# Optimization experiments

Hardware: AMD Instinct MI355X
Metric: run time of the kernel (lower is better)

The kernel has to match this reference:

```python
import jax, jax.numpy as jnp
from jax import lax
import numpy as np

B, T = 32, 64
E = 64        # embed_dim
U = 32        # num_measurements
D0, D1 = 300, 100
S = 9         # speaker_num
CELL = 64     # output_cell_dim
C = 6         # n_classes
EPS = 1e-12


def setup_inputs() -> dict:
    key = jax.random.key(0)
    ks = jax.random.split(key, 16)
    sc = 1.0 / np.sqrt(E)
    n = lambda i, shape, s=1.0: (jax.random.normal(ks[i], shape, jnp.float32) * s)
    return {
        "x0": n(0, (B, T, D0)),
        "x1": n(1, (B, T, D1)),
        "smask": jax.random.uniform(ks[2], (B, T, S), jnp.float32),
        "umask": jnp.ones((B, T), jnp.float32),
        "W_ih0": n(3, (4 * E, D0), sc), "W_hh0": n(4, (4 * E, E), sc),
        "b_ih0": n(5, (4 * E,), sc), "b_hh0": n(6, (4 * E,), sc),
        "W_ih1": n(7, (4 * E, D1), sc), "W_hh1": n(8, (4 * E, E), sc),
        "b_ih1": n(9, (4 * E,), sc), "b_hh1": n(10, (4 * E,), sc),
        "phase_table": jax.random.uniform(ks[11], (S, E), jnp.float32, -np.pi, np.pi),
        "meas_kernel": jax.random.uniform(ks[12], (U, E, 2), jnp.float32),
        "W1": n(13, (CELL, 2 * U), 0.1), "b1": jnp.zeros((CELL,), jnp.float32),
        "W2": n(14, (C, CELL), 0.1), "b2": jnp.zeros((C,), jnp.float32),
    }


def _lstm_tanh(x, um, Wih, Whh, bih, bhh):
    # torch.nn.LSTMCell (gate order i,f,g,o) + extra tanh applied to h each step;
    # the tanh-ed h is carried as the recurrent state (dropout = identity in eval).
    b, t, _ = x.shape
    e = Whh.shape[1]

    def step(carry, inp):
        h, c = carry
        xt, ut = inp
        g = (xt * ut[:, None]) @ Wih.T + bih + h @ Whh.T + bhh
        i, f, gg, o = jnp.split(g, 4, axis=-1)
        c = jax.nn.sigmoid(f) * c + jax.nn.sigmoid(i) * jnp.tanh(gg)
        h = jnp.tanh(jax.nn.sigmoid(o) * jnp.tanh(c))
        return (h, c), h

    h0 = jnp.zeros((b, e), x.dtype)
    _, hs = lax.scan(step, (h0, h0), (jnp.swapaxes(x, 0, 1), um.T))
    return jnp.swapaxes(hs, 0, 1)  # (B,T,E)


def _measure(amp, phase, kernel):
    # pure state v = cos(phase)*amp + i sin(phase)*amp; rho = |v><v|
    r = jnp.cos(phase) * amp
    im = jnp.sin(phase) * amp
    rho_r = jnp.einsum('bti,btj->btij', r, r) + jnp.einsum('bti,btj->btij', im, im)
    rho_i = jnp.einsum('bti,btj->btij', im, r) - jnp.einsum('bti,btj->btij', r, im)
    u = kernel.shape[0]
    norm = jnp.clip(jnp.linalg.norm(kernel.reshape(u, -1), axis=-1), EPS)
    kn = kernel / norm[:, None, None]
    kr, ki = kn[..., 0], kn[..., 1]
    Pr = jnp.einsum('ui,uj->uij', kr, kr) + jnp.einsum('ui,uj->uij', ki, ki)
    Pi = jnp.einsum('ui,uj->uij', ki, kr) - jnp.einsum('ui,uj->uij', kr, ki)
    return jnp.einsum('btij,uij->btu', rho_r, Pr) - jnp.einsum('btij,uij->btu', rho_i, Pi)


def reference(x0, x1, smask, umask, W_ih0, W_hh0, b_ih0, b_hh0,
              W_ih1, W_hh1, b_ih1, b_hh1, phase_table, meas_kernel,
              W1, b1, W2, b2):
    h0 = _lstm_tanh(x0, umask, W_ih0, W_hh0, b_ih0, b_hh0)
    h1 = _lstm_tanh(x1, umask, W_ih1, W_hh1, b_ih1, b_hh1)
    norm = lambda h: h / jnp.clip(jnp.linalg.norm(h, axis=-1, keepdims=True), EPS)
    phase = phase_table[jnp.argmax(smask, axis=-1)]  # (B,T,E); table shared by both modalities
    m = jnp.concatenate([_measure(norm(h0), phase, meas_kernel),
                         _measure(norm(h1), phase, meas_kernel)], axis=-1)
    hid = jax.nn.relu(m @ W1.T + b1)
    pred = jnp.tanh(hid @ W2.T + b2)
    return jax.nn.log_softmax(pred, axis=2)
```

## Files before the change

### kernel.cpp

```cpp
#include <hip/hip_runtime.h>

typedef unsigned short ushort_t;
typedef unsigned int uint_t;

__device__ __forceinline__ float bf2f(ushort_t v) {
  union { uint_t u; float f; } x; x.u = ((uint_t)v) << 16; return x.f;
}
__device__ __forceinline__ float lo16(uint_t u) {
  union { uint_t u; float f; } x; x.u = u << 16; return x.f;
}
__device__ __forceinline__ float hi16(uint_t u) {
  union { uint_t u; float f; } x; x.u = u & 0xffff0000u; return x.f;
}
__device__ __forceinline__ ushort_t f2bf(float f) {
  union { float f; uint_t u; } x; x.f = f;
  uint_t u = x.u;
  uint_t r = (u + 0x7fffu + ((u >> 16) & 1u)) >> 16;
  return (ushort_t)r;
}
__device__ __forceinline__ bool is_bf16(const void* um) {
  return *(const uint_t*)um == 0x3F803F80u;
}
__device__ __forceinline__ float ld_dual(const void* p, int i, bool isb) {
  return isb ? bf2f(((const ushort_t*)p)[i]) : ((const float*)p)[i];
}
__device__ __forceinline__ float fsig(float x) { return 1.f / (1.f + __expf(-x)); }
__device__ __forceinline__ float ftanh(float x) { return 2.f / (1.f + __expf(-2.f * x)) - 1.f; }

__device__ __forceinline__ float dpp_add_xor1(float v) {
  const int r = __builtin_amdgcn_update_dpp(0, __float_as_int(v), 0xB1, 0xF, 0xF, true);
  return v + __int_as_float(r);
}
__device__ __forceinline__ float dpp_add_xor2(float v) {
  const int r = __builtin_amdgcn_update_dpp(0, __float_as_int(v), 0x4E, 0xF, 0xF, true);
  return v + __int_as_float(r);
}

template <int D, bool ISB>
__device__ __forceinline__ void proj_body(
    const void* __restrict__ x, const void* __restrict__ um,
    const void* __restrict__ Wih, const void* __restrict__ bih,
    const void* __restrict__ bhh, float* __restrict__ xw, float* xs)
{
  const int tid = threadIdx.x;
  const int r0 = blockIdx.x * 8;
  for (int i = tid; i < 8 * D; i += 256) {
    const int r = i / D;
    xs[i] = ld_dual(x, r0 * D + i, ISB) * ld_dual(um, r0 + r, ISB);
  }
  __syncthreads();
  float acc[8];
#pragma unroll
  for (int r = 0; r < 8; ++r) acc[r] = 0.f;
#pragma unroll 5
  for (int k = 0; k < D; k += 4) {
    float w0, w1, w2, w3;
    if (ISB) {
      const ushort_t* wr = (const ushort_t*)Wih + tid * D;
      const uint2 wu = *(const uint2*)(wr + k);
      w0 = lo16(wu.x); w1 = hi16(wu.x); w2 = lo16(wu.y); w3 = hi16(wu.y);
    } else {
      const float* wr = (const float*)Wih + tid * D;
      const float4 wv = *(const float4*)(wr + k);
      w0 = wv.x; w1 = wv.y; w2 = wv.z; w3 = wv.w;
    }
#pragma unroll
    for (int r = 0; r < 8; ++r) {
      const float4 xv = *(const float4*)(xs + r * D + k);
      acc[r] = fmaf(xv.x, w0, acc[r]);
      acc[r] = fmaf(xv.y, w1, acc[r]);
      acc[r] = fmaf(xv.z, w2, acc[r]);
      acc[r] = fmaf(xv.w, w3, acc[r]);
    }
  }
  const float bias = ld_dual(bih, tid, ISB) + ld_dual(bhh, tid, ISB);
  const int pos = ((tid & 63) << 2) | (tid >> 6);
#pragma unroll
  for (int r = 0; r < 8; ++r)
    xw[(r0 + r) * 256 + pos] = acc[r] + bias;
}

__global__ __launch_bounds__(256) void proj_both(
    const void* __restrict__ x0, const void* __restrict__ x1,
    const void* __restrict__ um,
    const void* __restrict__ Wih0, const void* __restrict__ bih0,
    const void* __restrict__ bhh0,
    const void* __restrict__ Wih1, const void* __restrict__ bih1,
    const void* __restrict__ bhh1,
    float* __restrict__ xw0, float* __restrict__ xw1)
{
  __shared__ __align__(16) float xs[8 * 300];
  const bool isb = is_bf16(um);
  if (blockIdx.y == 0) {
    if (isb) proj_body<300, true>(x0, um, Wih0, bih0, bhh0, xw0, xs);
    else     proj_body<300, false>(x0, um, Wih0, bih0, bhh0, xw0, xs);
  } else {
    if (isb) proj_body<100, true>(x1, um, Wih1, bih1, bhh1, xw1, xs);
    else     proj_body<100, false>(x1, um, Wih1, bih1, bhh1, xw1, xs);
  }
}

__global__ __launch_bounds__(256, 1) void lstm_k(
    const float* __restrict__ xw0, const float* __restrict__ xw1,
    const void* __restrict__ Whh0, const void* __restrict__ Whh1,
    const void* __restrict__ um,
    float* __restrict__ h0r, float* __restrict__ h1r)
{
  __shared__ __align__(16) float xws[64 * 256];
  __shared__ __align__(16) float hist[65 * 64];

  const int bid = blockIdx.x;
  const int l = bid >> 5;
  const int b = bid & 31;
  const float* xw = (l ? xw1 : xw0) + b * 64 * 256;
  const void* Whh = (l ? Whh1 : Whh0);
  float* hr = (l ? h1r : h0r) + b * 64 * 64;
  const int tid = threadIdx.x;
  const int e = tid >> 2;
  const int q = tid & 3;
  const int k0 = q << 4;
  const bool isb = is_bf16(um);

  for (int i = tid; i < 4096; i += 256)
    *(float4*)(xws + i * 4) = *(const float4*)(xw + i * 4);
  if (tid < 64) hist[tid] = 0.f;

  float w[4][16];
  if (isb) {
#pragma unroll
    for (int t = 0; t < 4; ++t) {
      const ushort_t* wr = (const ushort_t*)Whh + (t * 64 + e) * 64 + k0;
#pragma unroll
      for (int j = 0; j < 16; j += 8) {
        const uint4 v = *(const uint4*)(wr + j);
        w[t][j + 0] = lo16(v.x); w[t][j + 1] = hi16(v.x);
        w[t][j + 2] = lo16(v.y); w[t][j + 3] = hi16(v.y);
        w[t][j + 4] = lo16(v.z); w[t][j + 5] = hi16(v.z);
        w[t][j + 6] = lo16(v.w); w[t][j + 7] = hi16(v.w);
      }
    }
  } else {
#pragma unroll
    for (int t = 0; t < 4; ++t) {
      const float* wr = (const float*)Whh + (t * 64 + e) * 64 + k0;
#pragma unroll
      for (int j = 0; j < 16; j += 4) {
        const float4 v = *(const float4*)(wr + j);
        w[t][j + 0] = v.x; w[t][j + 1] = v.y;
        w[t][j + 2] = v.z; w[t][j + 3] = v.w;
      }
    }
  }
  __syncthreads();

  float c = 0.f;
  for (int s = 0; s < 64; ++s) {
    const float gin = xws[s * 256 + tid];
    const float* hp = hist + s * 64 + k0;
    float p0 = 0.f, p1 = 0.f, p2 = 0.f, p3 = 0.f;
#pragma unroll
    for (int j = 0; j < 16; j += 4) {
      const float4 hv = *(const float4*)(hp + j);
      p0 = fmaf(w[0][j + 0], hv.x, p0); p0 = fmaf(w[0][j + 1], hv.y, p0);
      p0 = fmaf(w[0][j + 2], hv.z, p0); p0 = fmaf(w[0][j + 3], hv.w, p0);
      p1 = fmaf(w[1][j + 0], hv.x, p1); p1 = fmaf(w[1][j + 1], hv.y, p1);
      p1 = fmaf(w[1][j + 2], hv.z, p1); p1 = fmaf(w[1][j + 3], hv.w, p1);
      p2 = fmaf(w[2][j + 0], hv.x, p2); p2 = fmaf(w[2][j + 1], hv.y, p2);
      p2 = fmaf(w[2][j + 2], hv.z, p2); p2 = fmaf(w[2][j + 3], hv.w, p2);
      p3 = fmaf(w[3][j + 0], hv.x, p3); p3 = fmaf(w[3][j + 1], hv.y, p3);
      p3 = fmaf(w[3][j + 2], hv.z, p3); p3 = fmaf(w[3][j + 3], hv.w, p3);
    }
    if (q == 0) p0 += gin;
    else if (q == 1) p1 += gin;
    else if (q == 2) p2 += gin;
    else p3 += gin;
    p0 = dpp_add_xor1(p0); p0 = dpp_add_xor2(p0);
    p1 = dpp_add_xor1(p1); p1 = dpp_add_xor2(p1);
    p2 = dpp_add_xor1(p2); p2 = dpp_add_xor2(p2);
    p3 = dpp_add_xor1(p3); p3 = dpp_add_xor2(p3);
    const float yi = fsig(p0);
    const float yf = fsig(p1);
    const float yg = ftanh(p2);
    const float yo = fsig(p3);
    c = fmaf(yf, c, yi * yg);
    const float h = ftanh(yo * ftanh(c));
    if (q == 0) hist[(s + 1) * 64 + e] = h;
    __syncthreads();
  }
  for (int i = tid; i < 1024; i += 256)
    *(float4*)(hr + i * 4) = *(const float4*)(hist + 64 + i * 4);
}

__global__ __launch_bounds__(256) void head_k(
    const float* __restrict__ h0r, const float* __restrict__ h1r,
    const void* __restrict__ smask, const void* __restrict__ um,
    const void* __restrict__ ptab, const void* __restrict__ mker,
    const void* __restrict__ W1, const void* __restrict__ b1,
    const void* __restrict__ W2, const void* __restrict__ b2,
    void* __restrict__ out)
{
  __shared__ float2 knT[64][32];
  __shared__ float w1T[64][64];
  __shared__ float w2T[64][8];
  __shared__ float b1s[64];
  __shared__ float b2s[8];
  __shared__ float rim[4][4][64];
  __shared__ float msh[4][64];
  __shared__ float hidsh[4][64];
  __shared__ float psh[4][8];

  const int tid = threadIdx.x;
  const bool isb = is_bf16(um);
  {
    const int u = tid >> 3, sub = tid & 7;
    float vr[8], vi[8];
    float ssq = 0.f;
#pragma unroll
    for (int qq = 0; qq < 8; ++qq) {
      const int e = sub * 8 + qq;
      if (isb) {
        const uint_t kk = ((const uint_t*)mker)[u * 64 + e];
        vr[qq] = lo16(kk); vi[qq] = hi16(kk);
      } else {
        const float2 kk = ((const float2*)mker)[u * 64 + e];
        vr[qq] = kk.x; vi[qq] = kk.y;
      }
      ssq = fmaf(vr[qq], vr[qq], ssq);
      ssq = fmaf(vi[qq], vi[qq], ssq);
    }
    ssq += __shfl_xor(ssq, 1);
    ssq += __shfl_xor(ssq, 2);
    ssq += __shfl_xor(ssq, 4);
    const float rn = 1.f / fmaxf(sqrtf(ssq), 1e-12f);
#pragma unroll
    for (int qq = 0; qq < 8; ++qq) {
      const int e = sub * 8 + qq;
      knT[e][u] = make_float2(vr[qq] * rn, vi[qq] * rn);
    }
  }
  for (int i = tid; i < 4096; i += 256) {
    const int j = i >> 6, ll = i & 63;
    w1T[ll][j] = ld_dual(W1, i, isb);
  }
  if (tid < 64) b1s[tid] = ld_dual(b1, tid, isb);
  for (int i = tid; i < 384; i += 256) {
    const int cc = i >> 6, j = i & 63;
    w2T[j][cc] = ld_dual(W2, i, isb);
  }
  if (tid < 6) b2s[tid] = ld_dual(b2, tid, isb);
  __syncthreads();

  const int wv = tid >> 6, lane = tid & 63;
  const int item = blockIdx.x * 4 + wv;
  const float h0raw = h0r[item * 64 + lane];
  const float h1raw = h1r[item * 64 + lane];
  float ss0 = h0raw * h0raw, ss1 = h1raw * h1raw;
#pragma unroll
  for (int m = 1; m < 64; m <<= 1) {
    ss0 += __shfl_xor(ss0, m);
    ss1 += __shfl_xor(ss1, m);
  }
  const float h0 = h0raw / fmaxf(sqrtf(ss0), 1e-12f);
  const float h1 = h1raw / fmaxf(sqrtf(ss1), 1e-12f);

  int idx = 0;
  if (lane == 0) {
    float best = -1e30f;
#pragma unroll
    for (int si = 0; si < 9; ++si) {
      const float v = ld_dual(smask, item * 9 + si, isb);
      if (v > best) { best = v; idx = si; }
    }
  }
  idx = __shfl(idx, 0, 64);
  const float ph = ld_dual(ptab, idx * 64 + lane, isb);
  float sr, cr;
  __sincosf(ph, &sr, &cr);
  rim[wv][0][lane] = cr * h0;
  rim[wv][1][lane] = sr * h0;
  rim[wv][2][lane] = cr * h1;
  rim[wv][3][lane] = sr * h1;
  __syncthreads();
  {
    const int u = lane & 31;
    const float* ra = rim[wv][(lane >= 32) ? 2 : 0];
    const float* ia = rim[wv][(lane >= 32) ? 3 : 1];
    float ar = 0.f, ai = 0.f;
#pragma unroll 8
    for (int e = 0; e < 64; ++e) {
      const float2 k = knT[e][u];
      const float rr = ra[e], ii = ia[e];
      ar = fmaf(rr, k.x, ar);
      ar = fmaf(-ii, k.y, ar);
      ai = fmaf(rr, k.y, ai);
      ai = fmaf(ii, k.x, ai);
    }
    msh[wv][lane] = fmaf(ar, ar, ai * ai);
  }
  __syncthreads();
  {
    float acc = b1s[lane];
#pragma unroll 8
    for (int L = 0; L < 64; ++L)
      acc = fmaf(msh[wv][L], w1T[L][lane], acc);
    hidsh[wv][lane] = fmaxf(acc, 0.f);
  }
  __syncthreads();
  if (lane < 6) {
    float a2 = b2s[lane];
#pragma unroll 8
    for (int j = 0; j < 64; ++j)
      a2 = fmaf(hidsh[wv][j], w2T[j][lane], a2);
    psh[wv][lane] = ftanh(a2);
  }
  __syncthreads();
  if (lane < 6) {
    const float p = psh[wv][lane];
    float mx = psh[wv][0];
#pragma unroll
    for (int cc = 1; cc < 6; ++cc) mx = fmaxf(mx, psh[wv][cc]);
    float sum = 0.f;
#pragma unroll
    for (int cc = 0; cc < 6; ++cc) sum += __expf(psh[wv][cc] - mx);
    const float res = p - mx - __logf(sum);
    if (isb) ((ushort_t*)out)[item * 6 + lane] = f2bf(res);
    else     ((float*)out)[item * 6 + lane] = res;
  }
}

extern "C" void kernel_launch(void* const* d_in, const int* in_sizes, int n_in,
                              void* d_out, int out_size, void* d_ws, size_t ws_size,
                              hipStream_t stream)
{
  (void)in_sizes; (void)n_in; (void)out_size; (void)ws_size;
  const void* x0    = d_in[0];
  const void* x1    = d_in[1];
  const void* smask = d_in[2];
  const void* um    = d_in[3];
  const void* Wih0  = d_in[4];
  const void* Whh0  = d_in[5];
  const void* bih0  = d_in[6];
  const void* bhh0  = d_in[7];
  const void* Wih1  = d_in[8];
  const void* Whh1  = d_in[9];
  const void* bih1  = d_in[10];
  const void* bhh1  = d_in[11];
  const void* ptab  = d_in[12];
  const void* mker  = d_in[13];
  const void* W1    = d_in[14];
  const void* b1    = d_in[15];
  const void* W2    = d_in[16];
  const void* b2    = d_in[17];

  float* xw0 = (float*)d_ws;
  float* xw1 = xw0 + 2048 * 256;
  float* h0r = xw1 + 2048 * 256;
  float* h1r = h0r + 2048 * 64;

  hipLaunchKernelGGL(proj_both, dim3(256, 2), dim3(256), 0, stream,
                     x0, x1, um, Wih0, bih0, bhh0, Wih1, bih1, bhh1,
                     xw0, xw1);
  hipLaunchKernelGGL(lstm_k, dim3(64), dim3(256), 0, stream,
                     xw0, xw1, Whh0, Whh1, um, h0r, h1r);
  hipLaunchKernelGGL(head_k, dim3(512), dim3(256), 0, stream,
                     h0r, h1r, smask, um, ptab, mker, W1, b1, W2, b2,
                     d_out);
}
```

Baseline: 165.9 us.

## Use packed 2-wide FMA in LSTM and input projection, retile projection blocks

Rewrites the inner products of the recurrent LSTM step and the input projection to use 2-wide float vectors with an elementwise fma builtin, aiming for packed FP32 FMA instructions on CDNA. The projection kernel now uses 512-thread blocks covering 16 rows, with each thread computing two gate outputs over four rows, so fewer blocks are launched and each weight load is reused more. The head kernel's shared weight arrays are padded to avoid bank conflicts. Packed FMA changes the summation order slightly, and the larger projection blocks may lower occupancy.

```diff
diff --git a/kernel.cpp b/kernel.cpp
--- a/kernel.cpp
+++ b/kernel.cpp
@@ -2,6 +2,7 @@
 
 typedef unsigned short ushort_t;
 typedef unsigned int uint_t;
+typedef float f32x2 __attribute__((ext_vector_type(2)));
 
 __device__ __forceinline__ float bf2f(ushort_t v) {
   union { uint_t u; float f; } x; x.u = ((uint_t)v) << 16; return x.f;
@@ -27,6 +28,18 @@
 __device__ __forceinline__ float fsig(float x) { return 1.f / (1.f + __expf(-x)); }
 __device__ __forceinline__ float ftanh(float x) { return 2.f / (1.f + __expf(-2.f * x)) - 1.f; }
 
+#if defined(__has_builtin)
+#if __has_builtin(__builtin_elementwise_fma)
+#define FMA2(a, b, c) __builtin_elementwise_fma((a), (b), (c))
+#endif
+#endif
+#ifndef FMA2
+__device__ __forceinline__ f32x2 fma2_fb(f32x2 a, f32x2 b, f32x2 c) {
+  c.x = fmaf(a.x, b.x, c.x); c.y = fmaf(a.y, b.y, c.y); return c;
+}
+#define FMA2(a, b, c) fma2_fb((a), (b), (c))
+#endif
+
 __device__ __forceinline__ float dpp_add_xor1(float v) {
   const int r = __builtin_amdgcn_update_dpp(0, __float_as_int(v), 0xB1, 0xF, 0xF, true);
   return v + __int_as_float(r);
@@ -43,44 +56,59 @@
     const void* __restrict__ bhh, float* __restrict__ xw, float* xs)
 {
   const int tid = threadIdx.x;
-  const int r0 = blockIdx.x * 8;
-  for (int i = tid; i < 8 * D; i += 256) {
+  const int gp = tid & 127;
+  const int rg4 = (tid >> 7) << 2;
+  const int r0 = blockIdx.x * 16;
+  for (int i = tid; i < 16 * D; i += 512) {
     const int r = i / D;
     xs[i] = ld_dual(x, r0 * D + i, ISB) * ld_dual(um, r0 + r, ISB);
   }
   __syncthreads();
-  float acc[8];
-#pragma unroll
-  for (int r = 0; r < 8; ++r) acc[r] = 0.f;
+  f32x2 acc[2][4];
+#pragma unroll
+  for (int g = 0; g < 2; ++g)
+#pragma unroll
+    for (int r = 0; r < 4; ++r) acc[g][r] = f32x2{0.f, 0.f};
 #pragma unroll 5
   for (int k = 0; k < D; k += 4) {
-    float w0, w1, w2, w3;
+    f32x2 wA0, wA1, wB0, wB1;
     if (ISB) {
-      const ushort_t* wr = (const ushort_t*)Wih + tid * D;
-      const uint2 wu = *(const uint2*)(wr + k);
-      w0 = lo16(wu.x); w1 = hi16(wu.x); w2 = lo16(wu.y); w3 = hi16(wu.y);
+      const ushort_t* w0p = (const ushort_t*)Wih + (2 * gp) * D + k;
+      const uint2 u0 = *(const uint2*)w0p;
+      const uint2 u1 = *(const uint2*)(w0p + D);
+      wA0 = f32x2{lo16(u0.x), hi16(u0.x)}; wA1 = f32x2{lo16(u0.y), hi16(u0.y)};
+      wB0 = f32x2{lo16(u1.x), hi16(u1.x)}; wB1 = f32x2{lo16(u1.y), hi16(u1.y)};
     } else {
-      const float* wr = (const float*)Wih + tid * D;
-      const float4 wv = *(const float4*)(wr + k);
-      w0 = wv.x; w1 = wv.y; w2 = wv.z; w3 = wv.w;
-    }
-#pragma unroll
-    for (int r = 0; r < 8; ++r) {
-      const float4 xv = *(const float4*)(xs + r * D + k);
-      acc[r] = fmaf(xv.x, w0, acc[r]);
-      acc[r] = fmaf(xv.y, w1, acc[r]);
-      acc[r] = fmaf(xv.z, w2, acc[r]);
-      acc[r] = fmaf(xv.w, w3, acc[r]);
-    }
-  }
-  const float bias = ld_dual(bih, tid, ISB) + ld_dual(bhh, tid, ISB);
-  const int pos = ((tid & 63) << 2) | (tid >> 6);
-#pragma unroll
-  for (int r = 0; r < 8; ++r)
-    xw[(r0 + r) * 256 + pos] = acc[r] + bias;
-}
-
-__global__ __launch_bounds__(256) void proj_both(
+      const float* w0p = (const float*)Wih + (2 * gp) * D + k;
+      const float4 f0 = *(const float4*)w0p;
+      const float4 f1 = *(const float4*)(w0p + D);
+      wA0 = f32x2{f0.x, f0.y}; wA1 = f32x2{f0.z, f0.w};
+      wB0 = f32x2{f1.x, f1.y}; wB1 = f32x2{f1.z, f1.w};
+    }
+#pragma unroll
+    for (int r = 0; r < 4; ++r) {
+      const float4 xv = *(const float4*)(xs + (rg4 + r) * D + k);
+      const f32x2 xA = {xv.x, xv.y}, xB = {xv.z, xv.w};
+      acc[0][r] = FMA2(xA, wA0, acc[0][r]);
+      acc[0][r] = FMA2(xB, wA1, acc[0][r]);
+      acc[1][r] = FMA2(xA, wB0, acc[1][r]);
+      acc[1][r] = FMA2(xB, wB1, acc[1][r]);
+    }
+  }
+  const int g0 = 2 * gp, g1 = 2 * gp + 1;
+  const float b0 = ld_dual(bih, g0, ISB) + ld_dual(bhh, g0, ISB);
+  const float b1v = ld_dual(bih, g1, ISB) + ld_dual(bhh, g1, ISB);
+  const int pos0 = ((g0 & 63) << 2) | (g0 >> 6);
+  const int pos1 = ((g1 & 63) << 2) | (g1 >> 6);
+#pragma unroll
+  for (int r = 0; r < 4; ++r) {
+    const int row = r0 + rg4 + r;
+    xw[row * 256 + pos0] = acc[0][r].x + acc[0][r].y + b0;
+    xw[row * 256 + pos1] = acc[1][r].x + acc[1][r].y + b1v;
+  }
+}
+
+__global__ __launch_bounds__(512) void proj_both(
     const void* __restrict__ x0, const void* __restrict__ x1,
     const void* __restrict__ um,
     const void* __restrict__ Wih0, const void* __restrict__ bih0,
@@ -89,7 +117,7 @@
     const void* __restrict__ bhh1,
     float* __restrict__ xw0, float* __restrict__ xw1)
 {
-  __shared__ __align__(16) float xs[8 * 300];
+  __shared__ __align__(16) float xs[16 * 300];
   const bool isb = is_bf16(um);
   if (blockIdx.y == 0) {
     if (isb) proj_body<300, true>(x0, um, Wih0, bih0, bhh0, xw0, xs);
@@ -125,7 +153,7 @@
     *(float4*)(xws + i * 4) = *(const float4*)(xw + i * 4);
   if (tid < 64) hist[tid] = 0.f;
 
-  float w[4][16];
+  f32x2 w2[4][8];
   if (isb) {
 #pragma unroll
     for (int t = 0; t < 4; ++t) {
@@ -133,10 +161,10 @@
 #pragma unroll
       for (int j = 0; j < 16; j += 8) {
         const uint4 v = *(const uint4*)(wr + j);
-        w[t][j + 0] = lo16(v.x); w[t][j + 1] = hi16(v.x);
-        w[t][j + 2] = lo16(v.y); w[t][j + 3] = hi16(v.y);
-        w[t][j + 4] = lo16(v.z); w[t][j + 5] = hi16(v.z);
-        w[t][j + 6] = lo16(v.w); w[t][j + 7] = hi16(v.w);
+        w2[t][(j >> 1) + 0] = f32x2{lo16(v.x), hi16(v.x)};
+        w2[t][(j >> 1) + 1] = f32x2{lo16(v.y), hi16(v.y)};
+        w2[t][(j >> 1) + 2] = f32x2{lo16(v.z), hi16(v.z)};
+        w2[t][(j >> 1) + 3] = f32x2{lo16(v.w), hi16(v.w)};
       }
     }
   } else {
@@ -146,8 +174,8 @@
 #pragma unroll
       for (int j = 0; j < 16; j += 4) {
         const float4 v = *(const float4*)(wr + j);
-        w[t][j + 0] = v.x; w[t][j + 1] = v.y;
-        w[t][j + 2] = v.z; w[t][j + 3] = v.w;
+        w2[t][(j >> 1) + 0] = f32x2{v.x, v.y};
+        w2[t][(j >> 1) + 1] = f32x2{v.z, v.w};
       }
     }
   }
@@ -157,19 +185,21 @@
   for (int s = 0; s < 64; ++s) {
     const float gin = xws[s * 256 + tid];
     const float* hp = hist + s * 64 + k0;
-    float p0 = 0.f, p1 = 0.f, p2 = 0.f, p3 = 0.f;
+    f32x2 P0 = {0.f, 0.f}, P1 = {0.f, 0.f}, P2 = {0.f, 0.f}, P3 = {0.f, 0.f};
 #pragma unroll
     for (int j = 0; j < 16; j += 4) {
       const float4 hv = *(const float4*)(hp + j);
-      p0 = fmaf(w[0][j + 0], hv.x, p0); p0 = fmaf(w[0][j + 1], hv.y, p0);
-      p0 = fmaf(w[0][j + 2], hv.z, p0); p0 = fmaf(w[0][j + 3], hv.w, p0);
-      p1 = fmaf(w[1][j + 0], hv.x, p1); p1 = fmaf(w[1][j + 1], hv.y, p1);
-      p1 = fmaf(w[1][j + 2], hv.z, p1); p1 = fmaf(w[1][j + 3], hv.w, p1);
-      p2 = fmaf(w[2][j + 0], hv.x, p2); p2 = fmaf(w[2][j + 1], hv.y, p2);
-      p2 = fmaf(w[2][j + 2], hv.z, p2); p2 = fmaf(w[2][j + 3], hv.w, p2);
-      p3 = fmaf(w[3][j + 0], hv.x, p3); p3 = fmaf(w[3][j + 1], hv.y, p3);
-      p3 = fmaf(w[3][j + 2], hv.z, p3); p3 = fmaf(w[3][j + 3], hv.w, p3);
-    }
+      const f32x2 hA = {hv.x, hv.y}, hB = {hv.z, hv.w};
+      const int jp = j >> 1;
+      P0 = FMA2(w2[0][jp], hA, P0); P0 = FMA2(w2[0][jp + 1], hB, P0);
+      P1 = FMA2(w2[1][jp], hA, P1); P1 = FMA2(w2[1][jp + 1], hB, P1);
+      P2 = FMA2(w2[2][jp], hA, P2); P2 = FMA2(w2[2][jp + 1], hB, P2);
+      P3 = FMA2(w2[3][jp], hA, P3); P3 = FMA2(w2[3][jp + 1], hB, P3);
+    }
+    float p0 = P0.x + P0.y;
+    float p1 = P1.x + P1.y;
+    float p2 = P2.x + P2.y;
+    float p3 = P3.x + P3.y;
     if (q == 0) p0 += gin;
     else if (q == 1) p1 += gin;
     else if (q == 2) p2 += gin;
@@ -200,8 +230,8 @@
     void* __restrict__ out)
 {
   __shared__ float2 knT[64][32];
-  __shared__ float w1T[64][64];
-  __shared__ float w2T[64][8];
+  __shared__ float w1T[64][65];
+  __shared__ float w2T[64][9];
   __shared__ float b1s[64];
   __shared__ float b2s[8];
   __shared__ float rim[4][4][64];
@@ -357,7 +387,7 @@
   float* h0r = xw1 + 2048 * 256;
   float* h1r = h0r + 2048 * 64;
 
-  hipLaunchKernelGGL(proj_both, dim3(256, 2), dim3(256), 0, stream,
+  hipLaunchKernelGGL(proj_both, dim3(128, 2), dim3(512), 0, stream,
                      x0, x1, um, Wih0, bih0, bhh0, Wih1, bih1, bhh1,
                      xw0, xw1);
   hipLaunchKernelGGL(lstm_k, dim3(64), dim3(256), 0, stream,
```

After: 174.6 us. 5.2% more time.
